# Optimization experiments

Measured on AMD Instinct MI355X. Metric: run time of the kernel, lower is better.

## Reference

```python
import jax, jax.numpy as jnp
import numpy as np

B, M, N = 16, 128, 256
USER_DIM, ANT_DIM, EDGE_DIM = 8, 2, 1
HIDDEN, HEADS = 128, 4
HD = HIDDEN // HEADS
WB, DMIN, HZ, PMAX = 2.0, 0.01, 10.0, 1.0
SCALE = 1.0 / float(np.sqrt(HD))
NEG = 0.2  # leaky relu slope


def leaky(x):
    return jnp.where(x >= 0, x, NEG * x)


def ln(x, g, b, eps=1e-5):
    m = jnp.mean(x, axis=-1, keepdims=True)
    v = jnp.mean((x - m) ** 2, axis=-1, keepdims=True)
    return (x - m) * jax.lax.rsqrt(v + eps) * g + b


def setup_inputs() -> dict:
    key = jax.random.key(0)
    ks = jax.random.split(key, 16)
    rn = lambda k, shape, s: jax.random.normal(k, shape, jnp.float32) * s
    inp = {
        "user_feats": jax.random.normal(ks[0], (B, M, USER_DIM), jnp.float32),
        "ant_feats": jax.random.uniform(ks[1], (B, N, ANT_DIM), jnp.float32),
        "edge_feats": jax.random.uniform(ks[2], (B, M, N, EDGE_DIM), jnp.float32),
        # per-head projections (Linear no-bias) + their LayerNorm affine params
        "Wu": rn(ks[3], (HEADS, HD, USER_DIM), 0.5),
        "ln_u_g": jnp.ones((HEADS, HD)), "ln_u_b": jnp.zeros((HEADS, HD)),
        "Wa": rn(ks[4], (HEADS, HD, ANT_DIM), 0.5),
        "ln_a_g": jnp.ones((HEADS, HD)), "ln_a_b": jnp.zeros((HEADS, HD)),
        "We": rn(ks[5], (HEADS, HD, EDGE_DIM), 0.5),
        "ln_e_g": jnp.ones((HEADS, HD)), "ln_e_b": jnp.zeros((HEADS, HD)),
        "attn_v": rn(ks[6], (HEADS, HD), 0.5),
        # residual proj for antennas (the user residual branch is dead code in the block)
        "Wra": rn(ks[7], (HIDDEN, ANT_DIM), 0.5), "bra": jnp.zeros((HIDDEN,)),
        "ln_ant_g": jnp.ones((HIDDEN,)), "ln_ant_b": jnp.zeros((HIDDEN,)),
        # mlp_ant
        "Wm1": rn(ks[8], (HIDDEN // 2, HIDDEN), 0.1), "bm1": jnp.full((HIDDEN // 2,), 0.1),
        "Wm2": rn(ks[9], (2, HIDDEN // 2), 0.1), "bm2": jnp.full((2,), 0.1),
        # readouts over antenna axis
        "Wd1": rn(ks[10], (2 * N, N), 0.05), "bd1": jnp.zeros((2 * N,)),
        "Wd2": rn(ks[11], (N, 2 * N), 0.05), "bd2": jnp.zeros((N,)),
        "Wp1": rn(ks[12], (2 * N, N), 0.05), "bp1": jnp.zeros((2 * N,)),
        "Wp2": rn(ks[13], (N, 2 * N), 0.05), "bp2": jnp.zeros((N,)),
    }
    return inp


def reference(user_feats, ant_feats, edge_feats, Wu, ln_u_g, ln_u_b, Wa, ln_a_g, ln_a_b,
              We, ln_e_g, ln_e_b, attn_v, Wra, bra, ln_ant_g, ln_ant_b,
              Wm1, bm1, Wm2, bm2, Wd1, bd1, Wd2, bd2, Wp1, bp1, Wp2, bp2):
    # --- per-head bipartite attention (all heads batched on axis h) ---
    U = leaky(ln(jnp.einsum('bmi,hdi->hbmd', user_feats, Wu), ln_u_g[:, None, None, :], ln_u_b[:, None, None, :]))  # [h,B,M,hd]
    A = leaky(ln(jnp.einsum('bni,hdi->hbnd', ant_feats, Wa), ln_a_g[:, None, None, :], ln_a_b[:, None, None, :]))   # [h,B,N,hd]
    E = leaky(ln(jnp.einsum('bmni,hdi->hbmnd', edge_feats, We), ln_e_g[:, None, None, None, :], ln_e_b[:, None, None, None, :]))  # [h,B,M,N,hd]
    inter = leaky(U[:, :, :, None, :] + A[:, :, None, :, :] + E)                # [h,B,M,N,hd]
    scores = jnp.einsum('hbmnd,hd->hbmn', inter, attn_v) * SCALE
    alpha = jax.nn.softmax(scores, axis=-1)                                      # max-subtract softmax over N
    ant_out = jnp.einsum('hbmd,hbmn->hbnd', U, alpha)                            # [h,B,N,hd]
    ant_cat = jnp.transpose(ant_out, (1, 2, 0, 3)).reshape(B, N, HIDDEN)         # concat heads
    a_attn = jax.nn.relu(ant_cat + leaky(ant_feats @ Wra.T + bra))
    # --- block readouts ---
    a_attn = ln(a_attn, ln_ant_g, ln_ant_b)
    h1 = jax.nn.relu(a_attn @ Wm1.T + bm1)
    ant2d = jnp.clip(jax.nn.relu(h1 @ Wm2.T + bm2), -200.0, 200.0)               # [B,N,2]
    rd = jax.nn.relu(ant2d[..., 0] @ Wd1.T + bd1) @ Wd2.T + bd2                  # [B,N]
    rp = jax.nn.relu(ant2d[..., 1] @ Wp1.T + bp1) @ Wp2.T + bp2                  # [B,N]
    rd = jnp.clip(rd, 0.0, 100.0)
    rp = jnp.nan_to_num(rp, nan=0.0, posinf=1.0, neginf=0.0)
    # delta path
    Bmax = 2.0 * WB - (N - 1) * DMIN
    da = jax.nn.relu(rd)
    sd = jnp.sum(da, axis=1, keepdims=True)
    sdelta = jnp.clip((Bmax / jnp.maximum(Bmax, sd)) * da, 0.0, 100.0)
    idx = jnp.arange(N, dtype=sdelta.dtype)
    # closed form of the sequential recurrence x[n] = x[n-1] + sdelta[n] + DMIN - WB
    x = jnp.cumsum(sdelta, axis=1) + idx * DMIN - (idx + 1.0) * WB
    positions = jnp.stack([x, jnp.zeros_like(x), jnp.full_like(x, HZ)], axis=-1)  # [B,N,3]
    # power path
    eps = 1e-3
    pa = jnp.clip(jnp.nan_to_num(jax.nn.relu(rp), nan=0.0, posinf=1.0, neginf=0.0), 0.0, 1.0)
    sp = jnp.nan_to_num(jnp.sum(pa, axis=1, keepdims=True), nan=eps, posinf=eps, neginf=-eps)
    denom = jnp.maximum(sp, eps)
    sfp = jax.lax.stop_gradient(jnp.nan_to_num(PMAX / denom, nan=1.0, posinf=1.0, neginf=0.0))
    spow = jnp.clip(jnp.nan_to_num(sfp * pa, nan=0.0, posinf=1.0, neginf=0.0), 0.0, 1.0)
    ant_feats_out = jnp.stack([sdelta, spow], axis=-1)                            # [B,N,2]
    diff = user_feats[..., :2][:, :, None, :] - positions[:, None, :, :2]         # [B,M,N,2]
    edge_feats_new = jnp.sqrt(jnp.sum(diff * diff, axis=-1, keepdims=True))       # [B,M,N,1]
    return (ant_feats_out, edge_feats_new, positions)
```

## Files before the change

### kernel.cpp

```cpp
#include <hip/hip_runtime.h>
#include <math.h>

#define H_   4
#define HD_  32
#define B_   16
#define M_   128
#define N_   256
#define HID_ 128
#define MC_  8
#define MCH_ 16
#define SCALE_ 0.17677669529663687f

__device__ __forceinline__ float lrelu_f(float x) { return x >= 0.f ? x : 0.2f * x; }

__global__ __launch_bounds__(256) void k1_proj(
    const float* __restrict__ uf, const float* __restrict__ af,
    const float* __restrict__ Wu, const float* __restrict__ gu, const float* __restrict__ bu,
    const float* __restrict__ Wa, const float* __restrict__ ga, const float* __restrict__ ba,
    float* __restrict__ U, float* __restrict__ A)
{
  int row = blockIdx.x * 8 + (threadIdx.x >> 5);
  int d = threadIdx.x & 31;
  const int NU = H_ * B_ * M_;
  float x;
  const float* g; const float* bb; float* outp;
  if (row < NU) {
    int h = row >> 11, b = (row >> 7) & 15, m = row & 127;
    const float* in = uf + (b * M_ + m) * 8;
    const float* w  = Wu + (h * HD_ + d) * 8;
    x = 0.f;
    #pragma unroll
    for (int i = 0; i < 8; ++i) x = fmaf(in[i], w[i], x);
    g = gu + h * HD_; bb = bu + h * HD_;
    outp = U + (size_t)((h * B_ + b) * M_ + m) * HD_;
  } else {
    int r = row - NU;
    int h = r >> 12, b = (r >> 8) & 15, n = r & 255;
    const float* in = af + (b * N_ + n) * 2;
    const float* w  = Wa + (h * HD_ + d) * 2;
    x = fmaf(in[0], w[0], in[1] * w[1]);
    g = ga + h * HD_; bb = ba + h * HD_;
    outp = A + (size_t)((h * B_ + b) * N_ + n) * HD_;
  }
  float s = x;
  #pragma unroll
  for (int o = 16; o > 0; o >>= 1) s += __shfl_xor(s, o, 32);
  float mean = s * (1.f / 32.f);
  float df = x - mean;
  float v2 = df * df;
  #pragma unroll
  for (int o = 16; o > 0; o >>= 1) v2 += __shfl_xor(v2, o, 32);
  float y = df * rsqrtf(v2 * (1.f / 32.f) + 1e-5f) * g[d] + bb[d];
  outp[d] = lrelu_f(y);
}

__global__ __launch_bounds__(256) void k2_attn(
    const float* __restrict__ U, const float* __restrict__ A,
    const float* __restrict__ edge, const float* __restrict__ We,
    const float* __restrict__ ge, const float* __restrict__ be,
    const float* __restrict__ av, float* __restrict__ P)
{
  int blk = blockIdx.x;
  int h = blk & 3, b = (blk >> 2) & 15, mc = blk >> 6;
  int tid = threadIdx.x, n = tid;
  int lane = tid & 63, wid = tid >> 6;
  __shared__ float AB[N_ * 33];
  __shared__ float4 Ut4[HD_][4];
  __shared__ float4 cbv[HD_];
  __shared__ float red[4];
  __shared__ float vw_s;

  if (tid < 32) {
    int d = tid;
    float w = We[h * HD_ + d];
    float s = w;
    #pragma unroll
    for (int o = 16; o > 0; o >>= 1) s += __shfl_xor(s, o, 32);
    float mw = s * (1.f / 32.f);
    float df = w - mw;
    float v2 = df * df;
    #pragma unroll
    for (int o = 16; o > 0; o >>= 1) v2 += __shfl_xor(v2, o, 32);
    if (d == 0) vw_s = v2 * (1.f / 32.f);
    float vv = av[h * HD_ + d] * SCALE_;
    cbv[d] = make_float4(df * ge[h * HD_ + d], be[h * HD_ + d], 0.6f * vv, 0.4f * vv);
  }
  int m0 = mc * MCH_;
  for (int i = tid; i < MCH_ * HD_; i += 256) {
    int mm = i >> 5, d = i & 31;
    ((float*)Ut4)[d * 16 + mm] = U[(size_t)((h * B_ + b) * M_ + m0 + mm) * HD_ + d];
  }
  {
    const float4* ap = (const float4*)(A + (size_t)((h * B_ + b) * N_ + n) * HD_);
    #pragma unroll
    for (int i = 0; i < 8; ++i) {
      float4 t = ap[i];
      AB[n * 33 + 4 * i + 0] = t.x; AB[n * 33 + 4 * i + 1] = t.y;
      AB[n * 33 + 4 * i + 2] = t.z; AB[n * 33 + 4 * i + 3] = t.w;
    }
  }
  __syncthreads();
  float vw = vw_s;
  float tm[MCH_];
  #pragma unroll
  for (int mm = 0; mm < MCH_; ++mm) {
    float e = edge[(size_t)(b * M_ + m0 + mm) * N_ + n];
    tm[mm] = e * rsqrtf(fmaf(e * e, vw, 1e-5f));
  }
  float sc[MCH_];
  #pragma unroll
  for (int mm = 0; mm < MCH_; ++mm) sc[mm] = 0.f;
  const float* arow = &AB[n * 33];
  for (int d = 0; d < HD_; ++d) {
    float ad = arow[d];
    float4 qc = cbv[d];
    float4 u0 = Ut4[d][0], u1 = Ut4[d][1], u2 = Ut4[d][2], u3 = Ut4[d][3];
#define STEP(mi, uval) { float w_ = fmaf(tm[mi], qc.x, qc.y); \
    float E_ = fmaf(0.4f, fabsf(w_), 0.6f * w_); \
    float x_ = ad + uval + E_; \
    sc[mi] = fmaf(qc.z, x_, fmaf(qc.w, fabsf(x_), sc[mi])); }
    STEP(0, u0.x)  STEP(1, u0.y)  STEP(2, u0.z)  STEP(3, u0.w)
    STEP(4, u1.x)  STEP(5, u1.y)  STEP(6, u1.z)  STEP(7, u1.w)
    STEP(8, u2.x)  STEP(9, u2.y)  STEP(10, u2.z) STEP(11, u2.w)
    STEP(12, u3.x) STEP(13, u3.y) STEP(14, u3.z) STEP(15, u3.w)
#undef STEP
  }
  #pragma unroll 1
  for (int mm = 0; mm < MCH_; ++mm) {
    float v = sc[mm];
    #pragma unroll
    for (int o = 32; o > 0; o >>= 1) v = fmaxf(v, __shfl_xor(v, o, 64));
    if (lane == 0) red[wid] = v;
    __syncthreads();
    float mx = fmaxf(fmaxf(red[0], red[1]), fmaxf(red[2], red[3]));
    __syncthreads();
    float em = __expf(sc[mm] - mx);
    float s = em;
    #pragma unroll
    for (int o = 32; o > 0; o >>= 1) s += __shfl_xor(s, o, 64);
    if (lane == 0) red[wid] = s;
    __syncthreads();
    float tot = red[0] + red[1] + red[2] + red[3];
    __syncthreads();
    sc[mm] = em / tot;
  }
  float* accr = &AB[n * 33];
  for (int d = 0; d < HD_; ++d) {
    float4 u0 = Ut4[d][0], u1 = Ut4[d][1], u2 = Ut4[d][2], u3 = Ut4[d][3];
    float a0 = 0.f;
    a0 = fmaf(sc[0], u0.x, a0);  a0 = fmaf(sc[1], u0.y, a0);
    a0 = fmaf(sc[2], u0.z, a0);  a0 = fmaf(sc[3], u0.w, a0);
    a0 = fmaf(sc[4], u1.x, a0);  a0 = fmaf(sc[5], u1.y, a0);
    a0 = fmaf(sc[6], u1.z, a0);  a0 = fmaf(sc[7], u1.w, a0);
    a0 = fmaf(sc[8], u2.x, a0);  a0 = fmaf(sc[9], u2.y, a0);
    a0 = fmaf(sc[10], u2.z, a0); a0 = fmaf(sc[11], u2.w, a0);
    a0 = fmaf(sc[12], u3.x, a0); a0 = fmaf(sc[13], u3.y, a0);
    a0 = fmaf(sc[14], u3.z, a0); a0 = fmaf(sc[15], u3.w, a0);
    accr[d] = a0;
  }
  __syncthreads();
  float* Pbase = P + (size_t)((mc * 4 + h) * B_ + b) * (N_ * HD_);
  for (int i = tid; i < N_ * HD_; i += 256) {
    int nn = i >> 5, d = i & 31;
    Pbase[i] = AB[nn * 33 + d];
  }
}

__global__ __launch_bounds__(128) void k3_mlp(
    const float* __restrict__ P, const float* __restrict__ af,
    const float* __restrict__ Wra, const float* __restrict__ bra,
    const float* __restrict__ gant, const float* __restrict__ bant,
    const float* __restrict__ Wm1, const float* __restrict__ bm1,
    const float* __restrict__ Wm2, const float* __restrict__ bm2,
    float* __restrict__ rd_in, float* __restrict__ rp_in)
{
  int bn = blockIdx.x;
  int b = bn >> 8, n = bn & 255;
  int j = threadIdx.x;
  int lane = j & 63, wid = j >> 6;
  __shared__ float a2s[HID_];
  __shared__ float h1s[64];
  __shared__ float red[4];
  float cat = 0.f;
  #pragma unroll
  for (int mc = 0; mc < MC_; ++mc)
    cat += P[(size_t)((mc * 4 + (j >> 5)) * B_ + b) * (N_ * HD_) + n * HD_ + (j & 31)];
  float af0 = af[(b * N_ + n) * 2 + 0], af1 = af[(b * N_ + n) * 2 + 1];
  float r = fmaf(Wra[j * 2], af0, fmaf(Wra[j * 2 + 1], af1, bra[j]));
  float a1 = fmaxf(cat + lrelu_f(r), 0.f);
  float s = a1;
  #pragma unroll
  for (int o = 32; o > 0; o >>= 1) s += __shfl_xor(s, o, 64);
  if (lane == 0) red[wid] = s;
  __syncthreads();
  float mean = (red[0] + red[1]) * (1.f / 128.f);
  float df = a1 - mean;
  float v2 = df * df;
  #pragma unroll
  for (int o = 32; o > 0; o >>= 1) v2 += __shfl_xor(v2, o, 64);
  if (lane == 0) red[2 + wid] = v2;
  __syncthreads();
  float var = (red[2] + red[3]) * (1.f / 128.f);
  float a2 = df * rsqrtf(var + 1e-5f) * gant[j] + bant[j];
  a2s[j] = a2;
  __syncthreads();
  if (j < 64) {
    const float4* wr = (const float4*)(Wm1 + j * HID_);
    const float4* xs = (const float4*)a2s;
    float c0 = 0.f, c1 = 0.f, c2 = 0.f, c3 = 0.f;
    #pragma unroll
    for (int t = 0; t < 32; ++t) {
      float4 w = wr[t], x = xs[t];
      c0 = fmaf(w.x, x.x, c0); c1 = fmaf(w.y, x.y, c1);
      c2 = fmaf(w.z, x.z, c2); c3 = fmaf(w.w, x.w, c3);
    }
    h1s[j] = fmaxf((c0 + c1) + (c2 + c3) + bm1[j], 0.f);
  }
  __syncthreads();
  int c = wid;
  float p = h1s[lane] * Wm2[c * 64 + lane];
  #pragma unroll
  for (int o = 32; o > 0; o >>= 1) p += __shfl_xor(p, o, 64);
  if (lane == 0) {
    float v = p + bm2[c];
    v = fminf(fmaxf(v, 0.f), 200.f);
    (c == 0 ? rd_in : rp_in)[b * N_ + n] = v;
  }
}

__global__ __launch_bounds__(256) void k4a_l1(
    const float* __restrict__ rd_in, const float* __restrict__ rp_in,
    const float* __restrict__ Wd1, const float* __restrict__ bd1,
    const float* __restrict__ Wp1, const float* __restrict__ bp1,
    float* __restrict__ d1buf)
{
  int r = blockIdx.x * 4 + (threadIdx.x >> 6);
  int lane = threadIdx.x & 63;
  int path = r >> 13;
  int rem = r & 8191;
  int b = rem >> 9, i = rem & 511;
  const float* W = (path ? Wp1 : Wd1) + (size_t)i * N_;
  const float* bias = path ? bp1 : bd1;
  const float* x = (path ? rp_in : rd_in) + b * N_;
  float4 w = ((const float4*)W)[lane];
  float4 xv = ((const float4*)x)[lane];
  float s = fmaf(w.x, xv.x, fmaf(w.y, xv.y, fmaf(w.z, xv.z, w.w * xv.w)));
  #pragma unroll
  for (int o = 32; o > 0; o >>= 1) s += __shfl_xor(s, o, 64);
  if (lane == 0) d1buf[r] = fmaxf(s + bias[i], 0.f);
}

__global__ __launch_bounds__(256) void k4b_l2(
    const float* __restrict__ d1buf,
    const float* __restrict__ Wd2, const float* __restrict__ bd2,
    const float* __restrict__ Wp2, const float* __restrict__ bp2,
    float* __restrict__ rdbuf, float* __restrict__ rpbuf)
{
  int r = blockIdx.x * 4 + (threadIdx.x >> 6);
  int lane = threadIdx.x & 63;
  int path = r >> 12;
  int rem = r & 4095;
  int b = rem >> 8, n = rem & 255;
  const float* W = (path ? Wp2 : Wd2) + (size_t)n * (2 * N_);
  const float* x = d1buf + path * (B_ * 2 * N_) + b * (2 * N_);
  float4 w0 = ((const float4*)W)[lane * 2], w1 = ((const float4*)W)[lane * 2 + 1];
  float4 x0 = ((const float4*)x)[lane * 2], x1 = ((const float4*)x)[lane * 2 + 1];
  float s = fmaf(w0.x, x0.x, fmaf(w0.y, x0.y, fmaf(w0.z, x0.z, w0.w * x0.w)));
  s = fmaf(w1.x, x1.x, fmaf(w1.y, x1.y, fmaf(w1.z, x1.z, fmaf(w1.w, x1.w, s))));
  #pragma unroll
  for (int o = 32; o > 0; o >>= 1) s += __shfl_xor(s, o, 64);
  if (lane == 0) {
    if (path == 0) {
      float rd = s + bd2[n];
      rd = fminf(fmaxf(rd, 0.f), 100.f);
      rdbuf[b * N_ + n] = rd;
    } else {
      float rp = s + bp2[n];
      if (isnan(rp)) rp = 0.f;
      else if (isinf(rp)) rp = rp > 0.f ? 1.f : 0.f;
      float pa = fminf(fmaxf(rp, 0.f), 1.f);
      rpbuf[b * N_ + n] = pa;
    }
  }
}

__global__ __launch_bounds__(256) void k4c_final(
    const float* __restrict__ rdbuf, const float* __restrict__ rpbuf,
    float* __restrict__ out_af, float* __restrict__ out_pos, float* __restrict__ xbuf)
{
  int b = blockIdx.x;
  int q = threadIdx.x;
  int lane = q & 63, wid = q >> 6;
  __shared__ float red[8];
  float rd = rdbuf[b * N_ + q];
  float pa = rpbuf[b * N_ + q];
  float s = rd, s2 = pa;
  #pragma unroll
  for (int o = 32; o > 0; o >>= 1) { s += __shfl_xor(s, o, 64); s2 += __shfl_xor(s2, o, 64); }
  if (lane == 0) { red[wid] = s; red[4 + wid] = s2; }
  __syncthreads();
  float sd = red[0] + red[1] + red[2] + red[3];
  float sp = red[4] + red[5] + red[6] + red[7];
  const float Bmax = 2.f * 2.0f - (N_ - 1) * 0.01f;
  float f = Bmax / fmaxf(Bmax, sd);
  float sdelta = fminf(fmaxf(f * rd, 0.f), 100.f);
  float sfp = 1.0f / fmaxf(sp, 1e-3f);
  float spow = fminf(sfp * pa, 1.f);
  float val = sdelta;
  #pragma unroll
  for (int o = 1; o < 64; o <<= 1) {
    float t = __shfl_up(val, o, 64);
    if (lane >= o) val += t;
  }
  __syncthreads();
  if (lane == 63) red[wid] = val;
  __syncthreads();
  float off = 0.f;
  #pragma unroll
  for (int w2 = 0; w2 < 4; ++w2) if (w2 < wid) off += red[w2];
  float x = val + off + (float)q * 0.01f - (float)(q + 1) * 2.0f;
  out_af[(b * N_ + q) * 2 + 0] = sdelta;
  out_af[(b * N_ + q) * 2 + 1] = spow;
  out_pos[(b * N_ + q) * 3 + 0] = x;
  out_pos[(b * N_ + q) * 3 + 1] = 0.f;
  out_pos[(b * N_ + q) * 3 + 2] = 10.0f;
  xbuf[b * N_ + q] = x;
}

__global__ __launch_bounds__(256) void k5_edge(
    const float* __restrict__ uf, const float* __restrict__ xbuf,
    float* __restrict__ out_edge)
{
  int idx = blockIdx.x * 256 + threadIdx.x;
  int n = idx & 255, bm = idx >> 8;
  float u0 = uf[bm * 8 + 0], u1 = uf[bm * 8 + 1];
  float x = xbuf[(bm >> 7) * N_ + n];
  float dx = u0 - x;
  out_edge[idx] = sqrtf(fmaf(dx, dx, u1 * u1));
}

extern "C" void kernel_launch(void* const* d_in, const int* in_sizes, int n_in,
                              void* d_out, int out_size, void* d_ws, size_t ws_size,
                              hipStream_t stream) {
  (void)in_sizes; (void)n_in; (void)out_size; (void)ws_size;
  const float* uf   = (const float*)d_in[0];
  const float* af   = (const float*)d_in[1];
  const float* edge = (const float*)d_in[2];
  const float* Wu   = (const float*)d_in[3];
  const float* gu   = (const float*)d_in[4];
  const float* bu   = (const float*)d_in[5];
  const float* Wa   = (const float*)d_in[6];
  const float* ga   = (const float*)d_in[7];
  const float* ba   = (const float*)d_in[8];
  const float* We   = (const float*)d_in[9];
  const float* ge   = (const float*)d_in[10];
  const float* be   = (const float*)d_in[11];
  const float* av   = (const float*)d_in[12];
  const float* Wra  = (const float*)d_in[13];
  const float* bra  = (const float*)d_in[14];
  const float* gant = (const float*)d_in[15];
  const float* bant = (const float*)d_in[16];
  const float* Wm1  = (const float*)d_in[17];
  const float* bm1  = (const float*)d_in[18];
  const float* Wm2  = (const float*)d_in[19];
  const float* bm2  = (const float*)d_in[20];
  const float* Wd1  = (const float*)d_in[21];
  const float* bd1  = (const float*)d_in[22];
  const float* Wd2  = (const float*)d_in[23];
  const float* bd2  = (const float*)d_in[24];
  const float* Wp1  = (const float*)d_in[25];
  const float* bp1  = (const float*)d_in[26];
  const float* Wp2  = (const float*)d_in[27];
  const float* bp2  = (const float*)d_in[28];

  float* ws    = (float*)d_ws;
  float* U     = ws;
  float* A     = ws + 262144;
  float* P     = ws + 786432;
  float* rd_in = ws + 4980736;
  float* rp_in = ws + 4984832;
  float* d1buf = ws + 4988928;
  float* rdbuf = ws + 5005312;
  float* rpbuf = ws + 5009408;
  float* xbuf  = ws + 5013504;

  float* out      = (float*)d_out;
  float* out_af   = out;
  float* out_edge = out + 8192;
  float* out_pos  = out + 532480;

  hipLaunchKernelGGL(k1_proj, dim3(3072), dim3(256), 0, stream,
                     uf, af, Wu, gu, bu, Wa, ga, ba, U, A);
  hipLaunchKernelGGL(k2_attn, dim3(512), dim3(256), 0, stream,
                     U, A, edge, We, ge, be, av, P);
  hipLaunchKernelGGL(k3_mlp, dim3(4096), dim3(128), 0, stream,
                     P, af, Wra, bra, gant, bant, Wm1, bm1, Wm2, bm2, rd_in, rp_in);
  hipLaunchKernelGGL(k4a_l1, dim3(4096), dim3(256), 0, stream,
                     rd_in, rp_in, Wd1, bd1, Wp1, bp1, d1buf);
  hipLaunchKernelGGL(k4b_l2, dim3(2048), dim3(256), 0, stream,
                     d1buf, Wd2, bd2, Wp2, bp2, rdbuf, rpbuf);
  hipLaunchKernelGGL(k4c_final, dim3(16), dim3(256), 0, stream,
                     rdbuf, rpbuf, out_af, out_pos, xbuf);
  hipLaunchKernelGGL(k5_edge, dim3(2048), dim3(256), 0, stream,
                     uf, xbuf, out_edge);
}
```

Before: 186.1 us.

## Fuse projections into attention, batch softmax reductions, retile MLP, fold edge output

The per-head user/antenna projection and LayerNorm are now computed inside the attention kernel, which removes the k1 launch and the U/A workspace round trip. The softmax reductions are batched across all 16 rows so there are far fewer block barriers. The MLP kernel now handles 16 antennas per block with Wm1 staged in shared memory and vectorized P loads. The edge-distance kernel is folded into the final kernel. The catch is that each attention block recomputes its projections, and the edge output is written by only 16 blocks, which could leave it poorly parallelized.

```diff
diff --git a/kernel.cpp b/kernel.cpp
--- a/kernel.cpp
+++ b/kernel.cpp
@@ -6,58 +6,18 @@
 #define B_   16
 #define M_   128
 #define N_   256
-#define HID_ 128
 #define MC_  8
 #define MCH_ 16
 #define SCALE_ 0.17677669529663687f
 
 __device__ __forceinline__ float lrelu_f(float x) { return x >= 0.f ? x : 0.2f * x; }
 
-__global__ __launch_bounds__(256) void k1_proj(
+__global__ __launch_bounds__(256) void k2_attn(
     const float* __restrict__ uf, const float* __restrict__ af,
+    const float* __restrict__ edge,
     const float* __restrict__ Wu, const float* __restrict__ gu, const float* __restrict__ bu,
     const float* __restrict__ Wa, const float* __restrict__ ga, const float* __restrict__ ba,
-    float* __restrict__ U, float* __restrict__ A)
-{
-  int row = blockIdx.x * 8 + (threadIdx.x >> 5);
-  int d = threadIdx.x & 31;
-  const int NU = H_ * B_ * M_;
-  float x;
-  const float* g; const float* bb; float* outp;
-  if (row < NU) {
-    int h = row >> 11, b = (row >> 7) & 15, m = row & 127;
-    const float* in = uf + (b * M_ + m) * 8;
-    const float* w  = Wu + (h * HD_ + d) * 8;
-    x = 0.f;
-    #pragma unroll
-    for (int i = 0; i < 8; ++i) x = fmaf(in[i], w[i], x);
-    g = gu + h * HD_; bb = bu + h * HD_;
-    outp = U + (size_t)((h * B_ + b) * M_ + m) * HD_;
-  } else {
-    int r = row - NU;
-    int h = r >> 12, b = (r >> 8) & 15, n = r & 255;
-    const float* in = af + (b * N_ + n) * 2;
-    const float* w  = Wa + (h * HD_ + d) * 2;
-    x = fmaf(in[0], w[0], in[1] * w[1]);
-    g = ga + h * HD_; bb = ba + h * HD_;
-    outp = A + (size_t)((h * B_ + b) * N_ + n) * HD_;
-  }
-  float s = x;
-  #pragma unroll
-  for (int o = 16; o > 0; o >>= 1) s += __shfl_xor(s, o, 32);
-  float mean = s * (1.f / 32.f);
-  float df = x - mean;
-  float v2 = df * df;
-  #pragma unroll
-  for (int o = 16; o > 0; o >>= 1) v2 += __shfl_xor(v2, o, 32);
-  float y = df * rsqrtf(v2 * (1.f / 32.f) + 1e-5f) * g[d] + bb[d];
-  outp[d] = lrelu_f(y);
-}
-
-__global__ __launch_bounds__(256) void k2_attn(
-    const float* __restrict__ U, const float* __restrict__ A,
-    const float* __restrict__ edge, const float* __restrict__ We,
-    const float* __restrict__ ge, const float* __restrict__ be,
+    const float* __restrict__ We, const float* __restrict__ ge, const float* __restrict__ be,
     const float* __restrict__ av, float* __restrict__ P)
 {
   int blk = blockIdx.x;
@@ -67,7 +27,7 @@
   __shared__ float AB[N_ * 33];
   __shared__ float4 Ut4[HD_][4];
   __shared__ float4 cbv[HD_];
-  __shared__ float red[4];
+  __shared__ float wred[2][MCH_][4];
   __shared__ float vw_s;
 
   if (tid < 32) {
@@ -86,18 +46,42 @@
     cbv[d] = make_float4(df * ge[h * HD_ + d], be[h * HD_ + d], 0.6f * vv, 0.4f * vv);
   }
   int m0 = mc * MCH_;
-  for (int i = tid; i < MCH_ * HD_; i += 256) {
-    int mm = i >> 5, d = i & 31;
-    ((float*)Ut4)[d * 16 + mm] = U[(size_t)((h * B_ + b) * M_ + m0 + mm) * HD_ + d];
-  }
   {
-    const float4* ap = (const float4*)(A + (size_t)((h * B_ + b) * N_ + n) * HD_);
-    #pragma unroll
-    for (int i = 0; i < 8; ++i) {
-      float4 t = ap[i];
-      AB[n * 33 + 4 * i + 0] = t.x; AB[n * 33 + 4 * i + 1] = t.y;
-      AB[n * 33 + 4 * i + 2] = t.z; AB[n * 33 + 4 * i + 3] = t.w;
+    int m_loc = tid >> 4, s = tid & 15, dd = s * 2;
+    const float* urow = uf + (size_t)(b * M_ + m0 + m_loc) * 8;
+    const float* w0 = Wu + (h * HD_ + dd) * 8;
+    float x0 = 0.f, x1 = 0.f;
+    #pragma unroll
+    for (int i = 0; i < 8; ++i) { float u = urow[i]; x0 = fmaf(u, w0[i], x0); x1 = fmaf(u, w0[8 + i], x1); }
+    float sm = x0 + x1;
+    #pragma unroll
+    for (int o = 8; o > 0; o >>= 1) sm += __shfl_xor(sm, o, 64);
+    float mean = sm * (1.f / 32.f);
+    float d0 = x0 - mean, d1 = x1 - mean;
+    float vv = fmaf(d0, d0, d1 * d1);
+    #pragma unroll
+    for (int o = 8; o > 0; o >>= 1) vv += __shfl_xor(vv, o, 64);
+    float rs = rsqrtf(vv * (1.f / 32.f) + 1e-5f);
+    float y0 = fmaf(d0 * rs, gu[h * HD_ + dd],     bu[h * HD_ + dd]);
+    float y1 = fmaf(d1 * rs, gu[h * HD_ + dd + 1], bu[h * HD_ + dd + 1]);
+    ((float*)Ut4)[dd * 16 + m_loc]       = lrelu_f(y0);
+    ((float*)Ut4)[(dd + 1) * 16 + m_loc] = lrelu_f(y1);
+  }
+  {
+    float a0 = af[(b * N_ + n) * 2 + 0], a1 = af[(b * N_ + n) * 2 + 1];
+    float ar[HD_]; float sm = 0.f;
+    #pragma unroll
+    for (int d = 0; d < HD_; ++d) {
+      ar[d] = fmaf(a0, Wa[(h * HD_ + d) * 2], a1 * Wa[(h * HD_ + d) * 2 + 1]);
+      sm += ar[d];
     }
+    float mean = sm * (1.f / 32.f); float vv = 0.f;
+    #pragma unroll
+    for (int d = 0; d < HD_; ++d) { ar[d] -= mean; vv = fmaf(ar[d], ar[d], vv); }
+    float rs = rsqrtf(vv * (1.f / 32.f) + 1e-5f);
+    #pragma unroll
+    for (int d = 0; d < HD_; ++d)
+      AB[n * 33 + d] = lrelu_f(fmaf(ar[d] * rs, ga[h * HD_ + d], ba[h * HD_ + d]));
   }
   __syncthreads();
   float vw = vw_s;
@@ -125,25 +109,32 @@
     STEP(12, u3.x) STEP(13, u3.y) STEP(14, u3.z) STEP(15, u3.w)
 #undef STEP
   }
-  #pragma unroll 1
+  #pragma unroll
   for (int mm = 0; mm < MCH_; ++mm) {
     float v = sc[mm];
     #pragma unroll
     for (int o = 32; o > 0; o >>= 1) v = fmaxf(v, __shfl_xor(v, o, 64));
-    if (lane == 0) red[wid] = v;
-    __syncthreads();
-    float mx = fmaxf(fmaxf(red[0], red[1]), fmaxf(red[2], red[3]));
-    __syncthreads();
+    if (lane == 0) wred[0][mm][wid] = v;
+  }
+  __syncthreads();
+  #pragma unroll
+  for (int mm = 0; mm < MCH_; ++mm) {
+    float mx = fmaxf(fmaxf(wred[0][mm][0], wred[0][mm][1]),
+                     fmaxf(wred[0][mm][2], wred[0][mm][3]));
     float em = __expf(sc[mm] - mx);
-    float s = em;
-    #pragma unroll
-    for (int o = 32; o > 0; o >>= 1) s += __shfl_xor(s, o, 64);
-    if (lane == 0) red[wid] = s;
-    __syncthreads();
-    float tot = red[0] + red[1] + red[2] + red[3];
-    __syncthreads();
-    sc[mm] = em / tot;
-  }
+    sc[mm] = em;
+    float ss = em;
+    #pragma unroll
+    for (int o = 32; o > 0; o >>= 1) ss += __shfl_xor(ss, o, 64);
+    if (lane == 0) wred[1][mm][wid] = ss;
+  }
+  __syncthreads();
+  #pragma unroll
+  for (int mm = 0; mm < MCH_; ++mm) {
+    float tot = (wred[1][mm][0] + wred[1][mm][1]) + (wred[1][mm][2] + wred[1][mm][3]);
+    sc[mm] = sc[mm] / tot;
+  }
+  __syncthreads();
   float* accr = &AB[n * 33];
   for (int d = 0; d < HD_; ++d) {
     float4 u0 = Ut4[d][0], u1 = Ut4[d][1], u2 = Ut4[d][2], u3 = Ut4[d][3];
@@ -166,7 +157,7 @@
   }
 }
 
-__global__ __launch_bounds__(128) void k3_mlp(
+__global__ __launch_bounds__(256) void k3_mlp(
     const float* __restrict__ P, const float* __restrict__ af,
     const float* __restrict__ Wra, const float* __restrict__ bra,
     const float* __restrict__ gant, const float* __restrict__ bant,
@@ -174,57 +165,85 @@
     const float* __restrict__ Wm2, const float* __restrict__ bm2,
     float* __restrict__ rd_in, float* __restrict__ rp_in)
 {
-  int bn = blockIdx.x;
-  int b = bn >> 8, n = bn & 255;
-  int j = threadIdx.x;
-  int lane = j & 63, wid = j >> 6;
-  __shared__ float a2s[HID_];
-  __shared__ float h1s[64];
-  __shared__ float red[4];
-  float cat = 0.f;
-  #pragma unroll
-  for (int mc = 0; mc < MC_; ++mc)
-    cat += P[(size_t)((mc * 4 + (j >> 5)) * B_ + b) * (N_ * HD_) + n * HD_ + (j & 31)];
+  int b = blockIdx.x >> 4, nt = blockIdx.x & 15;
+  int tid = threadIdx.x;
+  int n_loc = tid >> 4, s = tid & 15;
+  int n = nt * 16 + n_loc;
+  int jj0 = s * 8;
+  int hh = s >> 2, d0 = (s & 3) * 8;
+  __shared__ float Wm1s[64][128];
+  __shared__ float a2s[16][128];
+  __shared__ float h1s[16][64];
+
+  {
+    const float4* wg = (const float4*)Wm1;
+    float4* wl = (float4*)Wm1s;
+    #pragma unroll
+    for (int k = 0; k < 8; ++k) wl[tid + 256 * k] = wg[tid + 256 * k];
+  }
+  float cat[8];
+  #pragma unroll
+  for (int k = 0; k < 8; ++k) cat[k] = 0.f;
+  #pragma unroll
+  for (int mc = 0; mc < MC_; ++mc) {
+    const float* base = P + (size_t)((mc * 4 + hh) * B_ + b) * (N_ * HD_) + n * HD_ + d0;
+    float4 p0 = ((const float4*)base)[0], p1 = ((const float4*)base)[1];
+    cat[0] += p0.x; cat[1] += p0.y; cat[2] += p0.z; cat[3] += p0.w;
+    cat[4] += p1.x; cat[5] += p1.y; cat[6] += p1.z; cat[7] += p1.w;
+  }
   float af0 = af[(b * N_ + n) * 2 + 0], af1 = af[(b * N_ + n) * 2 + 1];
-  float r = fmaf(Wra[j * 2], af0, fmaf(Wra[j * 2 + 1], af1, bra[j]));
-  float a1 = fmaxf(cat + lrelu_f(r), 0.f);
-  float s = a1;
-  #pragma unroll
-  for (int o = 32; o > 0; o >>= 1) s += __shfl_xor(s, o, 64);
-  if (lane == 0) red[wid] = s;
-  __syncthreads();
-  float mean = (red[0] + red[1]) * (1.f / 128.f);
-  float df = a1 - mean;
-  float v2 = df * df;
-  #pragma unroll
-  for (int o = 32; o > 0; o >>= 1) v2 += __shfl_xor(v2, o, 64);
-  if (lane == 0) red[2 + wid] = v2;
-  __syncthreads();
-  float var = (red[2] + red[3]) * (1.f / 128.f);
-  float a2 = df * rsqrtf(var + 1e-5f) * gant[j] + bant[j];
-  a2s[j] = a2;
-  __syncthreads();
-  if (j < 64) {
-    const float4* wr = (const float4*)(Wm1 + j * HID_);
-    const float4* xs = (const float4*)a2s;
+  float a1[8]; float sm = 0.f;
+  #pragma unroll
+  for (int k = 0; k < 8; ++k) {
+    int jj = jj0 + k;
+    float r = fmaf(Wra[jj * 2], af0, fmaf(Wra[jj * 2 + 1], af1, bra[jj]));
+    a1[k] = fmaxf(cat[k] + lrelu_f(r), 0.f);
+    sm += a1[k];
+  }
+  #pragma unroll
+  for (int o = 8; o > 0; o >>= 1) sm += __shfl_xor(sm, o, 64);
+  float mean = sm * (1.f / 128.f);
+  float vv = 0.f;
+  #pragma unroll
+  for (int k = 0; k < 8; ++k) { a1[k] -= mean; vv = fmaf(a1[k], a1[k], vv); }
+  #pragma unroll
+  for (int o = 8; o > 0; o >>= 1) vv += __shfl_xor(vv, o, 64);
+  float rs = rsqrtf(vv * (1.f / 128.f) + 1e-5f);
+  #pragma unroll
+  for (int k = 0; k < 8; ++k) {
+    int jj = jj0 + k;
+    a2s[n_loc][jj] = fmaf(a1[k] * rs, gant[jj], bant[jj]);
+  }
+  __syncthreads();
+  #pragma unroll
+  for (int k = 0; k < 4; ++k) {
+    int o = tid + 256 * k;
+    int row = o & 63, nl = o >> 6;
+    const float4* wr = (const float4*)Wm1s[row];
+    const float4* xr = (const float4*)a2s[nl];
     float c0 = 0.f, c1 = 0.f, c2 = 0.f, c3 = 0.f;
     #pragma unroll
-    for (int t = 0; t < 32; ++t) {
-      float4 w = wr[t], x = xs[t];
+    for (int c = 0; c < 32; ++c) {
+      int cc = (c + row) & 31;
+      float4 w = wr[cc], x = xr[cc];
       c0 = fmaf(w.x, x.x, c0); c1 = fmaf(w.y, x.y, c1);
       c2 = fmaf(w.z, x.z, c2); c3 = fmaf(w.w, x.w, c3);
     }
-    h1s[j] = fmaxf((c0 + c1) + (c2 + c3) + bm1[j], 0.f);
-  }
-  __syncthreads();
-  int c = wid;
-  float p = h1s[lane] * Wm2[c * 64 + lane];
-  #pragma unroll
-  for (int o = 32; o > 0; o >>= 1) p += __shfl_xor(p, o, 64);
-  if (lane == 0) {
-    float v = p + bm2[c];
-    v = fminf(fmaxf(v, 0.f), 200.f);
-    (c == 0 ? rd_in : rp_in)[b * N_ + n] = v;
+    h1s[nl][row] = fmaxf((c0 + c1) + (c2 + c3) + bm1[row], 0.f);
+  }
+  __syncthreads();
+  {
+    int c = s >> 3, e0 = (s & 7) * 8;
+    float p = 0.f;
+    #pragma unroll
+    for (int k = 0; k < 8; ++k) p = fmaf(h1s[n_loc][e0 + k], Wm2[c * 64 + e0 + k], p);
+    #pragma unroll
+    for (int o = 4; o > 0; o >>= 1) p += __shfl_xor(p, o, 64);
+    if ((s & 7) == 0) {
+      float v = p + bm2[c];
+      v = fminf(fmaxf(v, 0.f), 200.f);
+      (c == 0 ? rd_in : rp_in)[b * N_ + n] = v;
+    }
   }
 }
 
@@ -286,7 +305,8 @@
 
 __global__ __launch_bounds__(256) void k4c_final(
     const float* __restrict__ rdbuf, const float* __restrict__ rpbuf,
-    float* __restrict__ out_af, float* __restrict__ out_pos, float* __restrict__ xbuf)
+    const float* __restrict__ uf,
+    float* __restrict__ out_af, float* __restrict__ out_pos, float* __restrict__ out_edge)
 {
   int b = blockIdx.x;
   int q = threadIdx.x;
@@ -324,19 +344,12 @@
   out_pos[(b * N_ + q) * 3 + 0] = x;
   out_pos[(b * N_ + q) * 3 + 1] = 0.f;
   out_pos[(b * N_ + q) * 3 + 2] = 10.0f;
-  xbuf[b * N_ + q] = x;
-}
-
-__global__ __launch_bounds__(256) void k5_edge(
-    const float* __restrict__ uf, const float* __restrict__ xbuf,
-    float* __restrict__ out_edge)
-{
-  int idx = blockIdx.x * 256 + threadIdx.x;
-  int n = idx & 255, bm = idx >> 8;
-  float u0 = uf[bm * 8 + 0], u1 = uf[bm * 8 + 1];
-  float x = xbuf[(bm >> 7) * N_ + n];
-  float dx = u0 - x;
-  out_edge[idx] = sqrtf(fmaf(dx, dx, u1 * u1));
+  #pragma unroll 4
+  for (int m = 0; m < M_; ++m) {
+    float u0 = uf[(b * M_ + m) * 8 + 0], u1 = uf[(b * M_ + m) * 8 + 1];
+    float dx = u0 - x;
+    out_edge[(size_t)(b * M_ + m) * N_ + q] = sqrtf(fmaf(dx, dx, u1 * u1));
+  }
 }
 
 extern "C" void kernel_launch(void* const* d_in, const int* in_sizes, int n_in,
@@ -374,33 +387,26 @@
   const float* bp2  = (const float*)d_in[28];
 
   float* ws    = (float*)d_ws;
-  float* U     = ws;
-  float* A     = ws + 262144;
-  float* P     = ws + 786432;
-  float* rd_in = ws + 4980736;
-  float* rp_in = ws + 4984832;
-  float* d1buf = ws + 4988928;
-  float* rdbuf = ws + 5005312;
-  float* rpbuf = ws + 5009408;
-  float* xbuf  = ws + 5013504;
+  float* P     = ws;
+  float* rd_in = ws + 4194304;
+  float* rp_in = ws + 4198400;
+  float* d1buf = ws + 4202496;
+  float* rdbuf = ws + 4218880;
+  float* rpbuf = ws + 4222976;
 
   float* out      = (float*)d_out;
   float* out_af   = out;
   float* out_edge = out + 8192;
   float* out_pos  = out + 532480;
 
-  hipLaunchKernelGGL(k1_proj, dim3(3072), dim3(256), 0, stream,
-                     uf, af, Wu, gu, bu, Wa, ga, ba, U, A);
   hipLaunchKernelGGL(k2_attn, dim3(512), dim3(256), 0, stream,
-                     U, A, edge, We, ge, be, av, P);
-  hipLaunchKernelGGL(k3_mlp, dim3(4096), dim3(128), 0, stream,
+                     uf, af, edge, Wu, gu, bu, Wa, ga, ba, We, ge, be, av, P);
+  hipLaunchKernelGGL(k3_mlp, dim3(256), dim3(256), 0, stream,
                      P, af, Wra, bra, gant, bant, Wm1, bm1, Wm2, bm2, rd_in, rp_in);
   hipLaunchKernelGGL(k4a_l1, dim3(4096), dim3(256), 0, stream,
                      rd_in, rp_in, Wd1, bd1, Wp1, bp1, d1buf);
   hipLaunchKernelGGL(k4b_l2, dim3(2048), dim3(256), 0, stream,
                      d1buf, Wd2, bd2, Wp2, bp2, rdbuf, rpbuf);
   hipLaunchKernelGGL(k4c_final, dim3(16), dim3(256), 0, stream,
-                     rdbuf, rpbuf, out_af, out_pos, xbuf);
-  hipLaunchKernelGGL(k5_edge, dim3(2048), dim3(256), 0, stream,
-                     uf, xbuf, out_edge);
-}
+                     rdbuf, rpbuf, uf, out_af, out_pos, out_edge);
+}
```

Measured after the change: 183.5 us. About the same (-1.4%).
